# Optimization experiments

Hardware: AMD Instinct MI355X
Metric: run time of the kernel (lower is better)

The kernel has to match this reference:

```python
import jax, jax.numpy as jnp
import numpy as np

N = 100000   # nodes
D = 128      # embedding_dim
E = 1600000  # edges (avg in-degree 16)
L = 2        # num_layers
CURV = 1.0   # positive curvature (repo default -1.0 is NaN under sqrt)


def mobius_addition(x, y, c):
    xy = jnp.sum(x * y, axis=-1, keepdims=True)
    xn = jnp.sum(x * x, axis=-1, keepdims=True)
    yn = jnp.sum(y * y, axis=-1, keepdims=True)
    num = (1 + 2 * c * xy + c * yn) * x + (1 - c * xn) * y
    den = 1 + 2 * c * xy + c * c * xn * yn
    return num / den


def exp_map(x, v, c):
    vn = jnp.linalg.norm(v, axis=-1, keepdims=True)
    sc = jnp.sqrt(c)
    second = jnp.tanh(sc * vn / 2) * v / (sc * vn)
    return mobius_addition(x, second, c)


def log_map(x, y, c):
    add = mobius_addition(-x, y, c)
    an = jnp.linalg.norm(add, axis=-1, keepdims=True)
    sc = jnp.sqrt(c)
    return (2 / sc) * jnp.arctanh(sc * an) * add / an


def setup_inputs() -> dict:
    key = jax.random.key(0)
    ks = jax.random.split(key, 10)
    s = 1.0 / np.sqrt(D)  # torch Linear init scale
    embeddings = 0.01 * jax.random.normal(ks[0], (N, D), dtype=jnp.float32)  # ||x||<1 keeps atanh finite
    Wq = jax.random.uniform(ks[1], (L, D, D), jnp.float32, -s, s)
    bq = jax.random.uniform(ks[2], (L, D), jnp.float32, -s, s)
    Wk = jax.random.uniform(ks[3], (L, D, D), jnp.float32, -s, s)
    bk = jax.random.uniform(ks[4], (L, D), jnp.float32, -s, s)
    Wv = jax.random.uniform(ks[5], (L, D, D), jnp.float32, -s, s)
    bv = jax.random.uniform(ks[6], (L, D), jnp.float32, -s, s)
    src = jax.random.randint(ks[7], (E,), 0, N, dtype=jnp.int32)
    # guarantee every node has >=1 in-edge (DGL would leave isolated nodes at h=0 -> exp_map NaN)
    dst = jnp.concatenate([jnp.arange(N, dtype=jnp.int32),
                           jax.random.randint(ks[8], (E - N,), 0, N, dtype=jnp.int32)])
    curvature = jnp.array([CURV], dtype=jnp.float32)
    return {"embeddings": embeddings, "Wq": Wq, "bq": bq, "Wk": Wk, "bk": bk,
            "Wv": Wv, "bv": bv, "curvature": curvature, "src": src, "dst": dst}


def reference(embeddings, Wq, bq, Wk, bk, Wv, bv, curvature, src, dst):
    c = curvature  # shape [1], broadcasts against [..., 1]
    scale = float(D) ** 0.5
    x = embeddings
    origin = jnp.zeros((1, D), dtype=x.dtype)
    for l in range(Wq.shape[0]):
        t = log_map(origin, x, c)                      # [N, D] tangent at origin
        q = t @ Wq[l].T + bq[l]
        k = t @ Wk[l].T + bk[l]
        v = t @ Wv[l].T + bv[l]
        e = jnp.sum(k[src] * q[dst], axis=-1) / scale  # [E] edge scores
        m = jax.ops.segment_max(e, dst, num_segments=N)
        p = jnp.exp(e - m[dst])
        z = jax.ops.segment_sum(p, dst, num_segments=N)
        alpha = p / z[dst]                             # segment softmax over in-edges
        h = jax.ops.segment_sum(alpha[:, None] * v[src], dst, num_segments=N)
        x = exp_map(origin, h, c)
    return x
```

## Files before the change

### kernel.cpp

```cpp
#include <hip/hip_runtime.h>
#include <hip/hip_bf16.h>
#include <stdint.h>

typedef __attribute__((ext_vector_type(8))) short short8;
typedef __attribute__((ext_vector_type(4))) float f32x4;
typedef __attribute__((ext_vector_type(2))) float f32x2;
typedef __attribute__((ext_vector_type(4))) unsigned int u32x4;
typedef __attribute__((ext_vector_type(2))) _Float16 half2_t;

__device__ __forceinline__ uint32_t pack2(float a, float b) {
    auto r = __builtin_amdgcn_cvt_pkrtz(a, b);
    return __builtin_bit_cast(uint32_t, r);
}
__device__ __forceinline__ uint16_t f2h(float x) {
    auto r = __builtin_amdgcn_cvt_pkrtz(x, 0.0f);
    return (uint16_t)(__builtin_bit_cast(uint32_t, r) & 0xffffu);
}

__device__ __forceinline__ void agg_hist_add(int b, int lane, int* lcnt) {
    int prev = __shfl_up(b, 1);
    bool head = (lane == 0) || (b != prev);
    unsigned long long heads = __ballot(head);
    unsigned long long mask_le = ((1ull << lane) << 1) - 1ull;
    unsigned long long g = heads & ~mask_le;
    int nexthead = g ? (int)__builtin_ctzll(g) : 64;
    if (head && b >= 0) atomicAdd(&lcnt[b], nexthead - lane);
}
__device__ __forceinline__ int agg_slot(int b, int lane, int* cnt) {
    int prev = __shfl_up(b, 1);
    bool head = (lane == 0) || (b != prev);
    unsigned long long heads = __ballot(head);
    unsigned long long mask_le = ((1ull << lane) << 1) - 1ull;
    unsigned long long m = heads & mask_le;
    int myhead = 63 - (int)__builtin_clzll(m);
    unsigned long long g = heads & ~mask_le;
    int nexthead = g ? (int)__builtin_ctzll(g) : 64;
    int base = 0;
    if (lane == myhead && b >= 0) base = atomicAdd(&cnt[b], nexthead - lane);
    base = __shfl(base, myhead);
    return base + (lane - myhead);
}

#define DIM 128
#define BKT_SHIFT 7
#define BKT_NODES 128
#define MAX_BKT 1024
#define BIN_TILE 8192
#define CSR_CAP 3072
#define LDS_W_STRIDE 136
#define NW_BLK 16

__global__ __launch_bounds__(256) void prep_kernel(
    const int* __restrict__ dst, int* __restrict__ bucket_cnt, int* __restrict__ done_cnt,
    int* __restrict__ bstart, int* __restrict__ bcursor,
    int E, int nbuckets, int nbin,
    const float* __restrict__ Wq, const float* __restrict__ Wk, const float* __restrict__ Wv,
    uint16_t* __restrict__ w_h, int wtotal,
    const float* __restrict__ x, uint16_t* __restrict__ t, const float* __restrict__ curv,
    int N) {
    __shared__ int lcnt[MAX_BKT];
    __shared__ int is_last;
    int bx = blockIdx.x;
    int tid = threadIdx.x;
    if (bx < nbin) {
        for (int i = tid; i < nbuckets; i += 256) lcnt[i] = 0;
        __syncthreads();
        int base = bx * BIN_TILE;
        int end = min(base + BIN_TILE, E);
        int lane = tid & 63;
        for (int e0 = base; e0 < end; e0 += 256) {
            int e = e0 + tid;
            int b = (e < end) ? (dst[e] >> BKT_SHIFT) : -1;
            agg_hist_add(b, lane, lcnt);
        }
        __syncthreads();
        for (int i = tid; i < nbuckets; i += 256)
            if (lcnt[i]) atomicAdd(&bucket_cnt[i], lcnt[i]);
        if (tid == 0) {
            __threadfence();
            int d = atomicAdd(done_cnt, 1);
            is_last = (d == nbin - 1);
        }
        __syncthreads();
        if (is_last) {
            __threadfence();
            int v4[4];
            #pragma unroll
            for (int c = 0; c < 4; c++) {
                int idx = c * 256 + tid;
                v4[c] = (idx < nbuckets)
                    ? __hip_atomic_load(&bucket_cnt[idx], __ATOMIC_RELAXED, __HIP_MEMORY_SCOPE_AGENT)
                    : 0;
            }
            int run = 0;
            #pragma unroll
            for (int c = 0; c < 4; c++) {
                lcnt[tid] = v4[c]; __syncthreads();
                for (int off = 1; off < 256; off <<= 1) {
                    int tv = (tid >= off) ? lcnt[tid - off] : 0;
                    __syncthreads();
                    lcnt[tid] += tv;
                    __syncthreads();
                }
                int ex = run + lcnt[tid] - v4[c];
                int idx = c * 256 + tid;
                if (idx < nbuckets) { bstart[idx] = ex; bcursor[idx] = ex; }
                run += lcnt[255];
                __syncthreads();
            }
            if (tid == 0) bstart[nbuckets] = E;
        }
    } else if (bx < nbin + NW_BLK) {
        int per_l = 3 * DIM * DIM;
        for (int i = (bx - nbin) * 256 + tid; i < wtotal; i += 256 * NW_BLK) {
            int l = i / per_l;
            int rem = i % per_l;
            int mat = rem / (DIM * DIM);
            int idx = rem % (DIM * DIM);
            const float* s = (mat == 0) ? Wq : (mat == 1) ? Wk : Wv;
            w_h[i] = f2h(s[l * DIM * DIM + idx]);
        }
    } else {
        int n = (bx - nbin - NW_BLK) * 32 + (tid >> 3);
        if (n >= N) return;
        int ln8 = tid & 7;
        const float4* xp = (const float4*)(x + (size_t)n * DIM) + ln8 * 4;
        float4 a0 = xp[0], a1 = xp[1], a2 = xp[2], a3 = xp[3];
        float ss = a0.x * a0.x + a0.y * a0.y + a0.z * a0.z + a0.w * a0.w
                 + a1.x * a1.x + a1.y * a1.y + a1.z * a1.z + a1.w * a1.w
                 + a2.x * a2.x + a2.y * a2.y + a2.z * a2.z + a2.w * a2.w
                 + a3.x * a3.x + a3.y * a3.y + a3.z * a3.z + a3.w * a3.w;
        #pragma unroll
        for (int off = 4; off >= 1; off >>= 1) ss += __shfl_xor(ss, off);
        float c = curv[0];
        float sc = sqrtf(c);
        float r = sqrtf(ss);
        float z = sc * r;
        float f = (r > 1e-30f) ? __logf((1.0f + z) / (1.0f - z)) / (sc * r) : 2.0f;
        uint4 o0, o1;
        o0.x = pack2(f * a0.x, f * a0.y); o0.y = pack2(f * a0.z, f * a0.w);
        o0.z = pack2(f * a1.x, f * a1.y); o0.w = pack2(f * a1.z, f * a1.w);
        o1.x = pack2(f * a2.x, f * a2.y); o1.y = pack2(f * a2.z, f * a2.w);
        o1.z = pack2(f * a3.x, f * a3.y); o1.w = pack2(f * a3.z, f * a3.w);
        uint4* tp = (uint4*)(t + (size_t)n * DIM) + ln8 * 2;
        tp[0] = o0; tp[1] = o1;
    }
}

__device__ __forceinline__ void qkv_gemm_body(
    const uint16_t* __restrict__ t, const uint16_t* __restrict__ w,
    const float* __restrict__ bq, const float* __restrict__ bk, const float* __restrict__ bv,
    uint16_t* __restrict__ qout, uint8_t* __restrict__ k8out, uint16_t* __restrict__ vout,
    int N, int mat, int tile, uint16_t* lw) {
    const uint16_t* wm = w + (size_t)mat * DIM * DIM;
    {
        int r = threadIdx.x >> 1, hf = (threadIdx.x & 1) * 64;
        const uint4* srcp = (const uint4*)(wm + r * DIM + hf);
        uint4* dstp = (uint4*)(lw + r * LDS_W_STRIDE + hf);
        #pragma unroll
        for (int i = 0; i < 8; i++) dstp[i] = srcp[i];
    }
    __syncthreads();
    int wave = threadIdx.x >> 6, lane = threadIdx.x & 63;
    int sub = lane & 15, quad = lane >> 4;
    int node0 = tile * 256 + wave * 64;
    const float* bias = (mat == 0) ? bq : (mat == 1) ? bk : bv;
    f32x4 acc[8][4] = {};
    #pragma unroll
    for (int k0 = 0; k0 < DIM; k0 += 32) {
        short8 b[4];
        #pragma unroll
        for (int g = 0; g < 4; g++) {
            int node = node0 + g * 16 + sub;
            int nodec = (node < N) ? node : (N - 1);
            b[g] = *(const short8*)(t + (size_t)nodec * DIM + k0 + quad * 8);
        }
        short8 a[8];
        #pragma unroll
        for (int tl = 0; tl < 8; tl++)
            a[tl] = *(const short8*)(lw + (tl * 16 + sub) * LDS_W_STRIDE + k0 + quad * 8);
        #pragma unroll
        for (int tl = 0; tl < 8; tl++)
            #pragma unroll
            for (int g = 0; g < 4; g++)
                acc[tl][g] = __builtin_amdgcn_mfma_f32_16x16x32_f16(a[tl], b[g], acc[tl][g], 0, 0, 0);
    }
    #pragma unroll
    for (int g = 0; g < 4; g++) {
        int node = node0 + g * 16 + sub;
        if (node >= N) continue;
        if (mat == 1) {
            #pragma unroll
            for (int tl = 0; tl < 8; tl++) {
                float4 bs = *(const float4*)(bias + tl * 16 + quad * 4);
                int pk = 0;
                pk = __builtin_amdgcn_cvt_pk_fp8_f32(acc[tl][g][0] + bs.x, acc[tl][g][1] + bs.y, pk, false);
                pk = __builtin_amdgcn_cvt_pk_fp8_f32(acc[tl][g][2] + bs.z, acc[tl][g][3] + bs.w, pk, true);
                *(uint32_t*)(k8out + (size_t)node * DIM + tl * 16 + quad * 4) = (uint32_t)pk;
            }
        } else {
            uint16_t* outp = (mat == 0) ? qout : vout;
            #pragma unroll
            for (int tl = 0; tl < 8; tl++) {
                float4 bs = *(const float4*)(bias + tl * 16 + quad * 4);
                uint2 pk;
                pk.x = pack2(acc[tl][g][0] + bs.x, acc[tl][g][1] + bs.y);
                pk.y = pack2(acc[tl][g][2] + bs.z, acc[tl][g][3] + bs.w);
                *(uint2*)(outp + (size_t)node * DIM + tl * 16 + quad * 4) = pk;
            }
        }
    }
}

__global__ __launch_bounds__(256) void bin_gemm_kernel(
    const int* __restrict__ src, const int* __restrict__ dst,
    int* __restrict__ bcursor, int2* __restrict__ pair_buf, int E, int nbuckets, int nbin,
    const uint16_t* __restrict__ t, const uint16_t* __restrict__ w,
    const float* __restrict__ bq, const float* __restrict__ bk, const float* __restrict__ bv,
    uint16_t* __restrict__ qout, uint8_t* __restrict__ k8out, uint16_t* __restrict__ vout,
    int N, int ntiles) {
    __shared__ uint16_t lw[DIM * LDS_W_STRIDE];
    int bx = blockIdx.x;
    if (bx < nbin) {
        int* lcnt = (int*)lw;
        int* lbase = lcnt + MAX_BKT;
        int lane = threadIdx.x & 63;
        for (int i = threadIdx.x; i < nbuckets; i += 256) lcnt[i] = 0;
        __syncthreads();
        int base = bx * BIN_TILE;
        int end = min(base + BIN_TILE, E);
        for (int e0 = base; e0 < end; e0 += 256) {
            int e = e0 + threadIdx.x;
            int b = (e < end) ? (dst[e] >> BKT_SHIFT) : -1;
            agg_hist_add(b, lane, lcnt);
        }
        __syncthreads();
        for (int i = threadIdx.x; i < nbuckets; i += 256) {
            int c = lcnt[i];
            lbase[i] = c ? atomicAdd(&bcursor[i], c) : 0;
        }
        __syncthreads();
        for (int i = threadIdx.x; i < nbuckets; i += 256) lcnt[i] = 0;
        __syncthreads();
        for (int e0 = base; e0 < end; e0 += 256) {
            int e = e0 + threadIdx.x;
            bool valid = (e < end);
            int d = valid ? dst[e] : 0;
            int b = valid ? (d >> BKT_SHIFT) : -1;
            int slot = agg_slot(b, lane, lcnt);
            if (valid) pair_buf[(size_t)lbase[b] + slot] = make_int2(src[e], d);
        }
    } else {
        int id = bx - nbin;
        int mat = id / ntiles, tile = id % ntiles;
        qkv_gemm_body(t, w, bq, bk, bv, qout, k8out, vout, N, mat, tile, lw);
    }
}

__global__ __launch_bounds__(256) void qkv_gemm_kernel(
    const uint16_t* __restrict__ t, const uint16_t* __restrict__ w,
    const float* __restrict__ bq, const float* __restrict__ bk, const float* __restrict__ bv,
    uint16_t* __restrict__ qout, uint8_t* __restrict__ k8out, uint16_t* __restrict__ vout,
    int N) {
    __shared__ uint16_t lw[DIM * LDS_W_STRIDE];
    qkv_gemm_body(t, w, bq, bk, bv, qout, k8out, vout, N, blockIdx.y, blockIdx.x, lw);
}

__global__ __launch_bounds__(256) void csr_kernel(const int2* __restrict__ pair_buf,
                                                  const int* __restrict__ bstart,
                                                  int* __restrict__ row_start,
                                                  int* __restrict__ esrc,
                                                  int N, int E) {
    __shared__ int cnt[BKT_NODES], incl[BKT_NODES], cur[BKT_NODES];
    __shared__ int lsrc[CSR_CAP];
    int b = blockIdx.x;
    int node0 = b << BKT_SHIFT;
    int p0 = bstart[b], p1 = bstart[b + 1];
    int cntb = p1 - p0;
    int tid = threadIdx.x;
    if (tid < BKT_NODES) { cnt[tid] = 0; cur[tid] = 0; }
    __syncthreads();
    for (int i = p0 + tid; i < p1; i += 256)
        atomicAdd(&cnt[pair_buf[i].y & (BKT_NODES - 1)], 1);
    __syncthreads();
    if (tid < BKT_NODES) incl[tid] = cnt[tid];
    __syncthreads();
    for (int off = 1; off < BKT_NODES; off <<= 1) {
        int v = 0;
        if (tid < BKT_NODES && tid >= off) v = incl[tid - off];
        __syncthreads();
        if (tid < BKT_NODES) incl[tid] += v;
        __syncthreads();
    }
    if (tid < BKT_NODES) {
        int n = node0 + tid;
        if (n < N) row_start[n] = p0 + incl[tid] - cnt[tid];
    }
    if (b == 0 && tid == 0) row_start[N] = E;
    bool fit = (cntb <= CSR_CAP);
    __syncthreads();
    for (int i = p0 + tid; i < p1; i += 256) {
        int2 pr = pair_buf[i];
        int ln = pr.y & (BKT_NODES - 1);
        int slot = incl[ln] - cnt[ln] + atomicAdd(&cur[ln], 1);
        if (fit) lsrc[slot] = pr.x;
        else     esrc[p0 + slot] = pr.x;
    }
    __syncthreads();
    if (fit)
        for (int i = tid; i < cntb; i += 256) esrc[p0 + i] = lsrc[i];
}

__global__ __launch_bounds__(256) void attn_kernel(
    const uint16_t* __restrict__ q, const uint8_t* __restrict__ k8,
    const uint16_t* __restrict__ v,
    const int* __restrict__ row_start, const int* __restrict__ esrc,
    const float* __restrict__ curv,
    uint16_t* __restrict__ t_out,
    float* __restrict__ x_out,
    int N, int mode) {
    int wave = threadIdx.x >> 6, lane = threadIdx.x & 63;
    int sub = lane & 15, quad = lane >> 4;
    int n = blockIdx.x * 4 + wave;
    if (n >= N) return;
    int s0 = row_start[n], s1 = row_start[n + 1];
    u32x4 qu = __builtin_nontemporal_load((const u32x4*)(q + (size_t)n * DIM + sub * 8));
    f32x2 qf2[4];
    #pragma unroll
    for (int i = 0; i < 4; i++) {
        half2_t qh = __builtin_bit_cast(half2_t, qu[i]);
        qf2[i][0] = (float)qh.x; qf2[i][1] = (float)qh.y;
    }
    const float K2 = 0.12751744154470514f;
    float l = 0.0f;
    half2_t h2[4] = {};
    for (int s = s0; s < s1; s += 64) {
        int idx = s + lane;
        int sidx_all = __builtin_nontemporal_load(esrc + (idx < s1 ? idx : s1 - 1));
        int m = min(16, ((s1 - s) + 3) >> 2);
        for (int it0 = 0; it0 < m; it0 += 4) {
            uint2 ku[4]; uint4 vu[4];
            #pragma unroll
            for (int u = 0; u < 4; u++) {
                int sx = __shfl(sidx_all, (it0 + u) * 4 + quad);
                int ko = sx * DIM + sub * 8;
                ku[u] = *(const uint2*)(k8 + ko);
                vu[u] = *(const uint4*)(v + ko);
            }
            #pragma unroll
            for (int u = 0; u < 4; u++) {
                int e = s + (it0 + u) * 4 + quad;
                bool valid = (e < s1);
                f32x2 d0 = __builtin_amdgcn_cvt_pk_f32_fp8(ku[u].x, false);
                f32x2 d1 = __builtin_amdgcn_cvt_pk_f32_fp8(ku[u].x, true);
                f32x2 d2 = __builtin_amdgcn_cvt_pk_f32_fp8(ku[u].y, false);
                f32x2 d3 = __builtin_amdgcn_cvt_pk_f32_fp8(ku[u].y, true);
                f32x2 acc2 = qf2[0] * d0;
                acc2 += qf2[1] * d1;
                acc2 += qf2[2] * d2;
                acc2 += qf2[3] * d3;
                float dot = acc2[0] + acc2[1];
                #pragma unroll
                for (int off = 8; off >= 1; off >>= 1) dot += __shfl_xor(dot, off);
                float p = valid ? __builtin_amdgcn_exp2f(dot * K2) : 0.0f;
                l += p;
                _Float16 pf = (_Float16)p;
                half2_t ph = {pf, pf};
                #pragma unroll
                for (int i = 0; i < 4; i++) {
                    half2_t vh = __builtin_bit_cast(half2_t, ((const uint32_t*)&vu[u])[i]);
                    h2[i] += ph * vh;
                }
            }
        }
    }
    #pragma unroll
    for (int off = 16; off <= 32; off <<= 1) {
        l += __shfl_xor(l, off);
        #pragma unroll
        for (int i = 0; i < 4; i++) {
            uint32_t hw = __builtin_bit_cast(uint32_t, h2[i]);
            hw = __shfl_xor(hw, off);
            h2[i] += __builtin_bit_cast(half2_t, hw);
        }
    }
    float rl = 1.0f / l;
    if (mode == 0) {
        if (quad == 0) {
            _Float16 rlh = (_Float16)rl;
            half2_t rl2 = {rlh, rlh};
            uint4 pk;
            pk.x = __builtin_bit_cast(uint32_t, h2[0] * rl2);
            pk.y = __builtin_bit_cast(uint32_t, h2[1] * rl2);
            pk.z = __builtin_bit_cast(uint32_t, h2[2] * rl2);
            pk.w = __builtin_bit_cast(uint32_t, h2[3] * rl2);
            *(uint4*)(t_out + (size_t)n * DIM + sub * 8) = pk;
        }
    } else {
        float h[8];
        #pragma unroll
        for (int i = 0; i < 4; i++) {
            h[2 * i]     = (float)h2[i].x * rl;
            h[2 * i + 1] = (float)h2[i].y * rl;
        }
        float ss = 0.0f;
        #pragma unroll
        for (int j = 0; j < 8; j++) ss += h[j] * h[j];
        #pragma unroll
        for (int off = 8; off >= 1; off >>= 1) ss += __shfl_xor(ss, off);
        float c = curv[0];
        float sc = sqrtf(c);
        float nh = sqrtf(ss);
        float f = (nh > 1e-30f) ? tanhf(sc * nh * 0.5f) / (sc * nh) : 0.5f;
        if (quad == 0) {
            f32x4 o0 = {f * h[0], f * h[1], f * h[2], f * h[3]};
            f32x4 o1 = {f * h[4], f * h[5], f * h[6], f * h[7]};
            __builtin_nontemporal_store(o0, (f32x4*)(x_out + (size_t)n * DIM + sub * 8));
            __builtin_nontemporal_store(o1, (f32x4*)(x_out + (size_t)n * DIM + sub * 8 + 4));
        }
    }
}

extern "C" void kernel_launch(void* const* d_in, const int* in_sizes, int n_in,
                              void* d_out, int out_size, void* d_ws, size_t ws_size,
                              hipStream_t stream) {
    const float* emb  = (const float*)d_in[0];
    const float* Wq   = (const float*)d_in[1];
    const float* bq   = (const float*)d_in[2];
    const float* Wk   = (const float*)d_in[3];
    const float* bk   = (const float*)d_in[4];
    const float* Wv   = (const float*)d_in[5];
    const float* bv   = (const float*)d_in[6];
    const float* curv = (const float*)d_in[7];
    const int*   srcp = (const int*)d_in[8];
    const int*   dstp = (const int*)d_in[9];

    const int N = in_sizes[0] / DIM;
    const int L = in_sizes[2] / DIM;
    const int E = in_sizes[8];

    uint8_t* ws = (uint8_t*)d_ws;
    size_t off = 0;
    auto carve = [&](size_t bytes) { size_t o = off; off = (off + bytes + 255) & ~(size_t)255; return o; };
    uint16_t* t_buf   = (uint16_t*)(ws + carve((size_t)N * DIM * 2));
    uint16_t* qb      = (uint16_t*)(ws + carve((size_t)N * DIM * 2));
    uint16_t* vb      = (uint16_t*)(ws + carve((size_t)N * DIM * 2));
    uint8_t*  k8b     = (uint8_t*)(ws + carve((size_t)N * DIM));
    uint16_t* w_h     = (uint16_t*)(ws + carve((size_t)L * 3 * DIM * DIM * 2));
    int* row_start    = (int*)(ws + carve((size_t)(N + 1) * 4));
    int* bucket_cnt   = (int*)(ws + carve((MAX_BKT + 1) * 4));
    int* bstart       = (int*)(ws + carve((MAX_BKT + 1) * 4));
    int* bcursor      = (int*)(ws + carve(MAX_BKT * 4));
    int* esrc         = (int*)(ws + carve((size_t)E * 4));
    (void)ws_size;
    int* done_cnt = bucket_cnt + MAX_BKT;
    int2* pair_buf = (int2*)d_out;

    const int nbuckets = (N + BKT_NODES - 1) >> BKT_SHIFT;
    const int nbin = (E + BIN_TILE - 1) / BIN_TILE;
    const int wtotal = L * 3 * DIM * DIM;
    const int ntiles = (N + 255) / 256;

    (void)hipMemsetAsync(bucket_cnt, 0, (size_t)(MAX_BKT + 1) * 4, stream);
    int prep_grid = nbin + NW_BLK + (N + 31) / 32;
    prep_kernel<<<prep_grid, 256, 0, stream>>>(dstp, bucket_cnt, done_cnt, bstart, bcursor,
                                               E, nbuckets, nbin,
                                               Wq, Wk, Wv, w_h, wtotal,
                                               emb, t_buf, curv, N);
    bin_gemm_kernel<<<nbin + 3 * ntiles, 256, 0, stream>>>(
        srcp, dstp, bcursor, pair_buf, E, nbuckets, nbin,
        t_buf, w_h, bq, bk, bv, qb, k8b, vb, N, ntiles);
    csr_kernel<<<nbuckets, 256, 0, stream>>>(pair_buf, bstart, row_start, esrc, N, E);

    attn_kernel<<<(N + 3) / 4, 256, 0, stream>>>(
        qb, k8b, vb, row_start, esrc, curv, t_buf, (float*)d_out, N, (L == 1) ? 1 : 0);
    dim3 ggrid(ntiles, 3);
    for (int l = 1; l < L; l++) {
        qkv_gemm_kernel<<<ggrid, 256, 0, stream>>>(
            t_buf, w_h + (size_t)l * 3 * DIM * DIM,
            bq + (size_t)l * DIM, bk + (size_t)l * DIM, bv + (size_t)l * DIM,
            qb, k8b, vb, N);
        int mode = (l == L - 1) ? 1 : 0;
        attn_kernel<<<(N + 3) / 4, 256, 0, stream>>>(
            qb, k8b, vb, row_start, esrc, curv, t_buf, (float*)d_out, N, mode);
    }
}
```

Measured before the change: 453.5 us.

## Compute attention edge scores with FP8 MFMA and store Q in FP8

Q is now quantized to FP8 in the GEMM epilogue, halving its storage and load size. In the attention kernel, per-edge dot products that used to be scalar FP8-to-FP32 converts plus shuffle reductions are now done as 16x16x32 FP8 MFMAs over groups of 16 edges. The K gather switches from per-lane 8-byte chunks to per-row MFMA operand loads, and V gathers are re-indexed to match the MFMA output layout. This removes the cross-lane shuffle reductions, at the cost of lower Q precision and up to 15 wasted edge slots per group when in-degree is not a multiple of 16.

```diff
diff --git a/kernel.cpp b/kernel.cpp
--- a/kernel.cpp
+++ b/kernel.cpp
@@ -15,6 +15,10 @@
 __device__ __forceinline__ uint16_t f2h(float x) {
     auto r = __builtin_amdgcn_cvt_pkrtz(x, 0.0f);
     return (uint16_t)(__builtin_bit_cast(uint32_t, r) & 0xffffu);
+}
+__device__ __forceinline__ f32x4 mfma_fp8(uint2 a, uint2 b, f32x4 c) {
+    return __builtin_amdgcn_mfma_f32_16x16x32_fp8_fp8(
+        __builtin_bit_cast(long long, a), __builtin_bit_cast(long long, b), c, 0, 0, 0);
 }
 
 __device__ __forceinline__ void agg_hist_add(int b, int lane, int* lcnt) {
@@ -150,7 +154,7 @@
 __device__ __forceinline__ void qkv_gemm_body(
     const uint16_t* __restrict__ t, const uint16_t* __restrict__ w,
     const float* __restrict__ bq, const float* __restrict__ bk, const float* __restrict__ bv,
-    uint16_t* __restrict__ qout, uint8_t* __restrict__ k8out, uint16_t* __restrict__ vout,
+    uint8_t* __restrict__ q8out, uint8_t* __restrict__ k8out, uint16_t* __restrict__ vout,
     int N, int mat, int tile, uint16_t* lw) {
     const uint16_t* wm = w + (size_t)mat * DIM * DIM;
     {
@@ -189,24 +193,24 @@
     for (int g = 0; g < 4; g++) {
         int node = node0 + g * 16 + sub;
         if (node >= N) continue;
-        if (mat == 1) {
+        if (mat != 2) {
+            uint8_t* outp = (mat == 0) ? q8out : k8out;
             #pragma unroll
             for (int tl = 0; tl < 8; tl++) {
                 float4 bs = *(const float4*)(bias + tl * 16 + quad * 4);
                 int pk = 0;
                 pk = __builtin_amdgcn_cvt_pk_fp8_f32(acc[tl][g][0] + bs.x, acc[tl][g][1] + bs.y, pk, false);
                 pk = __builtin_amdgcn_cvt_pk_fp8_f32(acc[tl][g][2] + bs.z, acc[tl][g][3] + bs.w, pk, true);
-                *(uint32_t*)(k8out + (size_t)node * DIM + tl * 16 + quad * 4) = (uint32_t)pk;
+                *(uint32_t*)(outp + (size_t)node * DIM + tl * 16 + quad * 4) = (uint32_t)pk;
             }
         } else {
-            uint16_t* outp = (mat == 0) ? qout : vout;
             #pragma unroll
             for (int tl = 0; tl < 8; tl++) {
                 float4 bs = *(const float4*)(bias + tl * 16 + quad * 4);
                 uint2 pk;
                 pk.x = pack2(acc[tl][g][0] + bs.x, acc[tl][g][1] + bs.y);
                 pk.y = pack2(acc[tl][g][2] + bs.z, acc[tl][g][3] + bs.w);
-                *(uint2*)(outp + (size_t)node * DIM + tl * 16 + quad * 4) = pk;
+                *(uint2*)(vout + (size_t)node * DIM + tl * 16 + quad * 4) = pk;
             }
         }
     }
@@ -217,7 +221,7 @@
     int* __restrict__ bcursor, int2* __restrict__ pair_buf, int E, int nbuckets, int nbin,
     const uint16_t* __restrict__ t, const uint16_t* __restrict__ w,
     const float* __restrict__ bq, const float* __restrict__ bk, const float* __restrict__ bv,
-    uint16_t* __restrict__ qout, uint8_t* __restrict__ k8out, uint16_t* __restrict__ vout,
+    uint8_t* __restrict__ q8out, uint8_t* __restrict__ k8out, uint16_t* __restrict__ vout,
     int N, int ntiles) {
     __shared__ uint16_t lw[DIM * LDS_W_STRIDE];
     int bx = blockIdx.x;
@@ -253,17 +257,17 @@
     } else {
         int id = bx - nbin;
         int mat = id / ntiles, tile = id % ntiles;
-        qkv_gemm_body(t, w, bq, bk, bv, qout, k8out, vout, N, mat, tile, lw);
+        qkv_gemm_body(t, w, bq, bk, bv, q8out, k8out, vout, N, mat, tile, lw);
     }
 }
 
 __global__ __launch_bounds__(256) void qkv_gemm_kernel(
     const uint16_t* __restrict__ t, const uint16_t* __restrict__ w,
     const float* __restrict__ bq, const float* __restrict__ bk, const float* __restrict__ bv,
-    uint16_t* __restrict__ qout, uint8_t* __restrict__ k8out, uint16_t* __restrict__ vout,
+    uint8_t* __restrict__ q8out, uint8_t* __restrict__ k8out, uint16_t* __restrict__ vout,
     int N) {
     __shared__ uint16_t lw[DIM * LDS_W_STRIDE];
-    qkv_gemm_body(t, w, bq, bk, bv, qout, k8out, vout, N, blockIdx.y, blockIdx.x, lw);
+    qkv_gemm_body(t, w, bq, bk, bv, q8out, k8out, vout, N, blockIdx.y, blockIdx.x, lw);
 }
 
 __global__ __launch_bounds__(256) void csr_kernel(const int2* __restrict__ pair_buf,
@@ -312,7 +316,7 @@
 }
 
 __global__ __launch_bounds__(256) void attn_kernel(
-    const uint16_t* __restrict__ q, const uint8_t* __restrict__ k8,
+    const uint8_t* __restrict__ q8, const uint8_t* __restrict__ k8,
     const uint16_t* __restrict__ v,
     const int* __restrict__ row_start, const int* __restrict__ esrc,
     const float* __restrict__ curv,
@@ -324,51 +328,47 @@
     int n = blockIdx.x * 4 + wave;
     if (n >= N) return;
     int s0 = row_start[n], s1 = row_start[n + 1];
-    u32x4 qu = __builtin_nontemporal_load((const u32x4*)(q + (size_t)n * DIM + sub * 8));
-    f32x2 qf2[4];
-    #pragma unroll
-    for (int i = 0; i < 4; i++) {
-        half2_t qh = __builtin_bit_cast(half2_t, qu[i]);
-        qf2[i][0] = (float)qh.x; qf2[i][1] = (float)qh.y;
-    }
+    const uint8_t* qrow = q8 + (size_t)n * DIM;
+    uint2 qb0 = *(const uint2*)(qrow + quad * 8);
+    uint2 qb1 = *(const uint2*)(qrow + 32 + quad * 8);
+    uint2 qb2 = *(const uint2*)(qrow + 64 + quad * 8);
+    uint2 qb3 = *(const uint2*)(qrow + 96 + quad * 8);
     const float K2 = 0.12751744154470514f;
     float l = 0.0f;
     half2_t h2[4] = {};
     for (int s = s0; s < s1; s += 64) {
         int idx = s + lane;
         int sidx_all = __builtin_nontemporal_load(esrc + (idx < s1 ? idx : s1 - 1));
-        int m = min(16, ((s1 - s) + 3) >> 2);
-        for (int it0 = 0; it0 < m; it0 += 4) {
-            uint2 ku[4]; uint4 vu[4];
-            #pragma unroll
-            for (int u = 0; u < 4; u++) {
-                int sx = __shfl(sidx_all, (it0 + u) * 4 + quad);
-                int ko = sx * DIM + sub * 8;
-                ku[u] = *(const uint2*)(k8 + ko);
-                vu[u] = *(const uint4*)(v + ko);
-            }
-            #pragma unroll
-            for (int u = 0; u < 4; u++) {
-                int e = s + (it0 + u) * 4 + quad;
-                bool valid = (e < s1);
-                f32x2 d0 = __builtin_amdgcn_cvt_pk_f32_fp8(ku[u].x, false);
-                f32x2 d1 = __builtin_amdgcn_cvt_pk_f32_fp8(ku[u].x, true);
-                f32x2 d2 = __builtin_amdgcn_cvt_pk_f32_fp8(ku[u].y, false);
-                f32x2 d3 = __builtin_amdgcn_cvt_pk_f32_fp8(ku[u].y, true);
-                f32x2 acc2 = qf2[0] * d0;
-                acc2 += qf2[1] * d1;
-                acc2 += qf2[2] * d2;
-                acc2 += qf2[3] * d3;
-                float dot = acc2[0] + acc2[1];
-                #pragma unroll
-                for (int off = 8; off >= 1; off >>= 1) dot += __shfl_xor(dot, off);
-                float p = valid ? __builtin_amdgcn_exp2f(dot * K2) : 0.0f;
+        int ng = min(4, ((s1 - s) + 15) >> 4);
+        for (int g = 0; g < ng; g++) {
+            int kb = g * 16;
+            int ksrc = __shfl(sidx_all, kb + sub);
+            size_t ka = (size_t)ksrc * DIM + quad * 8;
+            uint2 a0 = *(const uint2*)(k8 + ka);
+            uint2 a1 = *(const uint2*)(k8 + ka + 32);
+            uint2 a2 = *(const uint2*)(k8 + ka + 64);
+            uint2 a3 = *(const uint2*)(k8 + ka + 96);
+            uint4 vu[4];
+            #pragma unroll
+            for (int r = 0; r < 4; r++) {
+                int vsrc = __shfl(sidx_all, kb + quad * 4 + r);
+                vu[r] = *(const uint4*)(v + (size_t)vsrc * DIM + sub * 8);
+            }
+            f32x4 d = {};
+            d = mfma_fp8(a0, qb0, d);
+            d = mfma_fp8(a1, qb1, d);
+            d = mfma_fp8(a2, qb2, d);
+            d = mfma_fp8(a3, qb3, d);
+            #pragma unroll
+            for (int r = 0; r < 4; r++) {
+                int e = s + kb + quad * 4 + r;
+                float p = (e < s1) ? __builtin_amdgcn_exp2f(d[r] * K2) : 0.0f;
                 l += p;
                 _Float16 pf = (_Float16)p;
                 half2_t ph = {pf, pf};
                 #pragma unroll
                 for (int i = 0; i < 4; i++) {
-                    half2_t vh = __builtin_bit_cast(half2_t, ((const uint32_t*)&vu[u])[i]);
+                    half2_t vh = __builtin_bit_cast(half2_t, ((const uint32_t*)&vu[r])[i]);
                     h2[i] += ph * vh;
                 }
             }
@@ -443,7 +443,7 @@
     size_t off = 0;
     auto carve = [&](size_t bytes) { size_t o = off; off = (off + bytes + 255) & ~(size_t)255; return o; };
     uint16_t* t_buf   = (uint16_t*)(ws + carve((size_t)N * DIM * 2));
-    uint16_t* qb      = (uint16_t*)(ws + carve((size_t)N * DIM * 2));
+    uint8_t*  q8b     = (uint8_t*)(ws + carve((size_t)N * DIM));
     uint16_t* vb      = (uint16_t*)(ws + carve((size_t)N * DIM * 2));
     uint8_t*  k8b     = (uint8_t*)(ws + carve((size_t)N * DIM));
     uint16_t* w_h     = (uint16_t*)(ws + carve((size_t)L * 3 * DIM * DIM * 2));
@@ -469,19 +469,19 @@
                                                emb, t_buf, curv, N);
     bin_gemm_kernel<<<nbin + 3 * ntiles, 256, 0, stream>>>(
         srcp, dstp, bcursor, pair_buf, E, nbuckets, nbin,
-        t_buf, w_h, bq, bk, bv, qb, k8b, vb, N, ntiles);
+        t_buf, w_h, bq, bk, bv, q8b, k8b, vb, N, ntiles);
     csr_kernel<<<nbuckets, 256, 0, stream>>>(pair_buf, bstart, row_start, esrc, N, E);
 
     attn_kernel<<<(N + 3) / 4, 256, 0, stream>>>(
-        qb, k8b, vb, row_start, esrc, curv, t_buf, (float*)d_out, N, (L == 1) ? 1 : 0);
+        q8b, k8b, vb, row_start, esrc, curv, t_buf, (float*)d_out, N, (L == 1) ? 1 : 0);
     dim3 ggrid(ntiles, 3);
     for (int l = 1; l < L; l++) {
         qkv_gemm_kernel<<<ggrid, 256, 0, stream>>>(
             t_buf, w_h + (size_t)l * 3 * DIM * DIM,
             bq + (size_t)l * DIM, bk + (size_t)l * DIM, bv + (size_t)l * DIM,
-            qb, k8b, vb, N);
+            q8b, k8b, vb, N);
         int mode = (l == L - 1) ? 1 : 0;
         attn_kernel<<<(N + 3) / 4, 256, 0, stream>>>(
-            qb, k8b, vb, row_start, esrc, curv, t_buf, (float*)d_out, N, mode);
-    }
-}
+            q8b, k8b, vb, row_start, esrc, curv, t_buf, (float*)d_out, N, mode);
+    }
+}
```

Measured after the change: 462.5 us. Within noise of the previous version (+2.0%).

## Store Q in fp8 and split QKV GEMM accumulators into two halves

Applied to the files above, without the earlier changes.

Q projections are now written as fp8 like K, which halves Q storage and the per-node Q read in the attention kernel. The GEMM body processes the output columns in two halves of four tiles each, so it needs fewer accumulator registers and may get better occupancy. The cost is lower precision for Q in the edge-score dot products and reloading the t operand twice.

```diff
diff --git a/kernel.cpp b/kernel.cpp
--- a/kernel.cpp
+++ b/kernel.cpp
@@ -6,6 +6,7 @@
 typedef __attribute__((ext_vector_type(4))) float f32x4;
 typedef __attribute__((ext_vector_type(2))) float f32x2;
 typedef __attribute__((ext_vector_type(4))) unsigned int u32x4;
+typedef __attribute__((ext_vector_type(2))) unsigned int u32x2;
 typedef __attribute__((ext_vector_type(2))) _Float16 half2_t;
 
 __device__ __forceinline__ uint32_t pack2(float a, float b) {
@@ -150,7 +151,7 @@
 __device__ __forceinline__ void qkv_gemm_body(
     const uint16_t* __restrict__ t, const uint16_t* __restrict__ w,
     const float* __restrict__ bq, const float* __restrict__ bk, const float* __restrict__ bv,
-    uint16_t* __restrict__ qout, uint8_t* __restrict__ k8out, uint16_t* __restrict__ vout,
+    uint8_t* __restrict__ q8out, uint8_t* __restrict__ k8out, uint16_t* __restrict__ vout,
     int N, int mat, int tile, uint16_t* lw) {
     const uint16_t* wm = w + (size_t)mat * DIM * DIM;
     {
@@ -165,48 +166,45 @@
     int sub = lane & 15, quad = lane >> 4;
     int node0 = tile * 256 + wave * 64;
     const float* bias = (mat == 0) ? bq : (mat == 1) ? bk : bv;
-    f32x4 acc[8][4] = {};
-    #pragma unroll
-    for (int k0 = 0; k0 < DIM; k0 += 32) {
-        short8 b[4];
+    for (int half = 0; half < 2; half++) {
+        f32x4 acc[4][4] = {};
+        #pragma unroll
+        for (int k0 = 0; k0 < DIM; k0 += 32) {
+            short8 b[4];
+            #pragma unroll
+            for (int g = 0; g < 4; g++) {
+                int node = node0 + g * 16 + sub;
+                int nodec = (node < N) ? node : (N - 1);
+                b[g] = *(const short8*)(t + (size_t)nodec * DIM + k0 + quad * 8);
+            }
+            #pragma unroll
+            for (int tl = 0; tl < 4; tl++) {
+                short8 a = *(const short8*)(lw + ((half * 4 + tl) * 16 + sub) * LDS_W_STRIDE + k0 + quad * 8);
+                #pragma unroll
+                for (int g = 0; g < 4; g++)
+                    acc[tl][g] = __builtin_amdgcn_mfma_f32_16x16x32_f16(a, b[g], acc[tl][g], 0, 0, 0);
+            }
+        }
         #pragma unroll
         for (int g = 0; g < 4; g++) {
             int node = node0 + g * 16 + sub;
-            int nodec = (node < N) ? node : (N - 1);
-            b[g] = *(const short8*)(t + (size_t)nodec * DIM + k0 + quad * 8);
-        }
-        short8 a[8];
-        #pragma unroll
-        for (int tl = 0; tl < 8; tl++)
-            a[tl] = *(const short8*)(lw + (tl * 16 + sub) * LDS_W_STRIDE + k0 + quad * 8);
-        #pragma unroll
-        for (int tl = 0; tl < 8; tl++)
-            #pragma unroll
-            for (int g = 0; g < 4; g++)
-                acc[tl][g] = __builtin_amdgcn_mfma_f32_16x16x32_f16(a[tl], b[g], acc[tl][g], 0, 0, 0);
-    }
-    #pragma unroll
-    for (int g = 0; g < 4; g++) {
-        int node = node0 + g * 16 + sub;
-        if (node >= N) continue;
-        if (mat == 1) {
-            #pragma unroll
-            for (int tl = 0; tl < 8; tl++) {
-                float4 bs = *(const float4*)(bias + tl * 16 + quad * 4);
-                int pk = 0;
-                pk = __builtin_amdgcn_cvt_pk_fp8_f32(acc[tl][g][0] + bs.x, acc[tl][g][1] + bs.y, pk, false);
-                pk = __builtin_amdgcn_cvt_pk_fp8_f32(acc[tl][g][2] + bs.z, acc[tl][g][3] + bs.w, pk, true);
-                *(uint32_t*)(k8out + (size_t)node * DIM + tl * 16 + quad * 4) = (uint32_t)pk;
-            }
-        } else {
-            uint16_t* outp = (mat == 0) ? qout : vout;
-            #pragma unroll
-            for (int tl = 0; tl < 8; tl++) {
-                float4 bs = *(const float4*)(bias + tl * 16 + quad * 4);
-                uint2 pk;
-                pk.x = pack2(acc[tl][g][0] + bs.x, acc[tl][g][1] + bs.y);
-                pk.y = pack2(acc[tl][g][2] + bs.z, acc[tl][g][3] + bs.w);
-                *(uint2*)(outp + (size_t)node * DIM + tl * 16 + quad * 4) = pk;
+            if (node >= N) continue;
+            #pragma unroll
+            for (int tl = 0; tl < 4; tl++) {
+                int tlg = half * 4 + tl;
+                float4 bs = *(const float4*)(bias + tlg * 16 + quad * 4);
+                if (mat != 2) {
+                    uint8_t* outp = (mat == 0) ? q8out : k8out;
+                    int pk = 0;
+                    pk = __builtin_amdgcn_cvt_pk_fp8_f32(acc[tl][g][0] + bs.x, acc[tl][g][1] + bs.y, pk, false);
+                    pk = __builtin_amdgcn_cvt_pk_fp8_f32(acc[tl][g][2] + bs.z, acc[tl][g][3] + bs.w, pk, true);
+                    *(uint32_t*)(outp + (size_t)node * DIM + tlg * 16 + quad * 4) = (uint32_t)pk;
+                } else {
+                    uint2 pk;
+                    pk.x = pack2(acc[tl][g][0] + bs.x, acc[tl][g][1] + bs.y);
+                    pk.y = pack2(acc[tl][g][2] + bs.z, acc[tl][g][3] + bs.w);
+                    *(uint2*)(vout + (size_t)node * DIM + tlg * 16 + quad * 4) = pk;
+                }
             }
         }
     }
@@ -217,7 +215,7 @@
     int* __restrict__ bcursor, int2* __restrict__ pair_buf, int E, int nbuckets, int nbin,
     const uint16_t* __restrict__ t, const uint16_t* __restrict__ w,
     const float* __restrict__ bq, const float* __restrict__ bk, const float* __restrict__ bv,
-    uint16_t* __restrict__ qout, uint8_t* __restrict__ k8out, uint16_t* __restrict__ vout,
+    uint8_t* __restrict__ q8out, uint8_t* __restrict__ k8out, uint16_t* __restrict__ vout,
     int N, int ntiles) {
     __shared__ uint16_t lw[DIM * LDS_W_STRIDE];
     int bx = blockIdx.x;
@@ -253,17 +251,17 @@
     } else {
         int id = bx - nbin;
         int mat = id / ntiles, tile = id % ntiles;
-        qkv_gemm_body(t, w, bq, bk, bv, qout, k8out, vout, N, mat, tile, lw);
+        qkv_gemm_body(t, w, bq, bk, bv, q8out, k8out, vout, N, mat, tile, lw);
     }
 }
 
 __global__ __launch_bounds__(256) void qkv_gemm_kernel(
     const uint16_t* __restrict__ t, const uint16_t* __restrict__ w,
     const float* __restrict__ bq, const float* __restrict__ bk, const float* __restrict__ bv,
-    uint16_t* __restrict__ qout, uint8_t* __restrict__ k8out, uint16_t* __restrict__ vout,
+    uint8_t* __restrict__ q8out, uint8_t* __restrict__ k8out, uint16_t* __restrict__ vout,
     int N) {
     __shared__ uint16_t lw[DIM * LDS_W_STRIDE];
-    qkv_gemm_body(t, w, bq, bk, bv, qout, k8out, vout, N, blockIdx.y, blockIdx.x, lw);
+    qkv_gemm_body(t, w, bq, bk, bv, q8out, k8out, vout, N, blockIdx.y, blockIdx.x, lw);
 }
 
 __global__ __launch_bounds__(256) void csr_kernel(const int2* __restrict__ pair_buf,
@@ -312,7 +310,7 @@
 }
 
 __global__ __launch_bounds__(256) void attn_kernel(
-    const uint16_t* __restrict__ q, const uint8_t* __restrict__ k8,
+    const uint8_t* __restrict__ q8, const uint8_t* __restrict__ k8,
     const uint16_t* __restrict__ v,
     const int* __restrict__ row_start, const int* __restrict__ esrc,
     const float* __restrict__ curv,
@@ -324,13 +322,12 @@
     int n = blockIdx.x * 4 + wave;
     if (n >= N) return;
     int s0 = row_start[n], s1 = row_start[n + 1];
-    u32x4 qu = __builtin_nontemporal_load((const u32x4*)(q + (size_t)n * DIM + sub * 8));
+    u32x2 qv = __builtin_nontemporal_load((const u32x2*)(q8 + (size_t)n * DIM + sub * 8));
     f32x2 qf2[4];
-    #pragma unroll
-    for (int i = 0; i < 4; i++) {
-        half2_t qh = __builtin_bit_cast(half2_t, qu[i]);
-        qf2[i][0] = (float)qh.x; qf2[i][1] = (float)qh.y;
-    }
+    qf2[0] = __builtin_amdgcn_cvt_pk_f32_fp8(qv[0], false);
+    qf2[1] = __builtin_amdgcn_cvt_pk_f32_fp8(qv[0], true);
+    qf2[2] = __builtin_amdgcn_cvt_pk_f32_fp8(qv[1], false);
+    qf2[3] = __builtin_amdgcn_cvt_pk_f32_fp8(qv[1], true);
     const float K2 = 0.12751744154470514f;
     float l = 0.0f;
     half2_t h2[4] = {};
@@ -443,7 +440,7 @@
     size_t off = 0;
     auto carve = [&](size_t bytes) { size_t o = off; off = (off + bytes + 255) & ~(size_t)255; return o; };
     uint16_t* t_buf   = (uint16_t*)(ws + carve((size_t)N * DIM * 2));
-    uint16_t* qb      = (uint16_t*)(ws + carve((size_t)N * DIM * 2));
+    uint8_t*  q8b     = (uint8_t*)(ws + carve((size_t)N * DIM));
     uint16_t* vb      = (uint16_t*)(ws + carve((size_t)N * DIM * 2));
     uint8_t*  k8b     = (uint8_t*)(ws + carve((size_t)N * DIM));
     uint16_t* w_h     = (uint16_t*)(ws + carve((size_t)L * 3 * DIM * DIM * 2));
@@ -469,19 +466,19 @@
                                                emb, t_buf, curv, N);
     bin_gemm_kernel<<<nbin + 3 * ntiles, 256, 0, stream>>>(
         srcp, dstp, bcursor, pair_buf, E, nbuckets, nbin,
-        t_buf, w_h, bq, bk, bv, qb, k8b, vb, N, ntiles);
+        t_buf, w_h, bq, bk, bv, q8b, k8b, vb, N, ntiles);
     csr_kernel<<<nbuckets, 256, 0, stream>>>(pair_buf, bstart, row_start, esrc, N, E);
 
     attn_kernel<<<(N + 3) / 4, 256, 0, stream>>>(
-        qb, k8b, vb, row_start, esrc, curv, t_buf, (float*)d_out, N, (L == 1) ? 1 : 0);
+        q8b, k8b, vb, row_start, esrc, curv, t_buf, (float*)d_out, N, (L == 1) ? 1 : 0);
     dim3 ggrid(ntiles, 3);
     for (int l = 1; l < L; l++) {
         qkv_gemm_kernel<<<ggrid, 256, 0, stream>>>(
             t_buf, w_h + (size_t)l * 3 * DIM * DIM,
             bq + (size_t)l * DIM, bk + (size_t)l * DIM, bv + (size_t)l * DIM,
-            qb, k8b, vb, N);
+            q8b, k8b, vb, N);
         int mode = (l == L - 1) ? 1 : 0;
         attn_kernel<<<(N + 3) / 4, 256, 0, stream>>>(
-            qb, k8b, vb, row_start, esrc, curv, t_buf, (float*)d_out, N, mode);
-    }
-}
+            q8b, k8b, vb, row_start, esrc, curv, t_buf, (float*)d_out, N, mode);
+    }
+}
```

New measurement: 442.8 us. 1.02x faster.
